# Kernel tuning notes

Measured on AMD Instinct MI355X. Metric: run time of the kernel, lower is better.

The kernel has to match this reference:

```python
import jax, jax.numpy as jnp
import numpy as np

B, N, D, R = 4, 192, 128, 32


def _sh_l1(r):
    # e3nn l=1 real SH with 'integral' normalization: sqrt(3/4pi) * r_hat
    rh = r / (jnp.linalg.norm(r, axis=-1, keepdims=True) + 1e-12)
    return np.sqrt(3.0 / (4.0 * np.pi)).astype(np.float32) * rh


def _sh_l2(r):
    # l=2 real SH of unit vector, integral normalization, standard m=-2..2 order
    rh = r / (jnp.linalg.norm(r, axis=-1, keepdims=True) + 1e-12)
    x, y, z = rh[..., 0], rh[..., 1], rh[..., 2]
    c = np.float32(0.5 / np.sqrt(np.pi))
    s15 = np.float32(np.sqrt(15.0))
    s5h = np.float32(0.5 * np.sqrt(5.0))
    return c * jnp.stack([s15 * x * y, s15 * y * z, s5h * (3.0 * z * z - 1.0),
                          s15 * x * z, 0.5 * s15 * (x * x - y * y)], axis=-1)


def _radial(x, W1, b1, W2, b2):
    return jax.nn.silu(x @ W1 + b1) @ W2 + b2


def _forward(node_s, node_v, node_t, rbf, r_hat, mask,
             Ws1, bs1, Ws2, bs2, Wd1, bd1, Wd2, bd2,
             Wv1, bv1, Wv2, bv2, Wt1, bt1, Wt2, bt2,
             ln_g, ln_b, Wo, bo, v_scale, t_scale):
    m = mask[..., None]                      # (B,N,N,1)
    Y1 = _sh_l1(r_hat)                       # (B,N,N,3)
    Y2 = _sh_l2(r_hat)                       # (B,N,N,5)
    # scalar messages: h_j[b,i,j,d] = node_s[b,j,d]*mask; w0 also masked (mask applied twice, as in source)
    w0 = _radial(rbf, Ws1, bs1, Ws2, bs2) * m
    msg_s = jnp.einsum('bjd,bij,bijd->bid', node_s, mask, w0)
    # vector->scalar channel: source broadcasts node_v over j via unsqueeze(2), i.e. uses node_v of center i
    dot_vY = jnp.einsum('bimd,bijm->bijd', node_v, Y1)     # (B,N,N,D)
    w110 = _radial(rbf, Wd1, bd1, Wd2, bd2) * m
    msg_s_from_v = jnp.sum(dot_vY * w110, axis=2)          # (B,N,D)
    # CG tensor product 0e x SH -> irrep with per-channel radial weight, masked twice
    m2 = (mask * mask)[..., None]
    sj = node_s[:, None, :, :]                             # (B,1,N,D) -> broadcast over i
    wv = _radial(rbf, Wv1, bv1, Wv2, bv2)
    delta_v = jnp.einsum('bijd,bijm->bimd', m2 * wv * sj, Y1)   # (B,N,3,D)
    wt = _radial(rbf, Wt1, bt1, Wt2, bt2)
    delta_t = jnp.einsum('bijd,bijm->bimd', m2 * wt * sj, Y2)   # (B,N,5,D)
    # output scalar head: LayerNorm + Linear
    x = msg_s + msg_s_from_v
    mu = jnp.mean(x, axis=-1, keepdims=True)
    var = jnp.var(x, axis=-1, keepdims=True)
    delta_s = ((x - mu) / jnp.sqrt(var + 1e-5) * ln_g + ln_b) @ Wo + bo
    return delta_s, delta_v * v_scale, delta_t * t_scale


def setup_inputs() -> dict:
    ks = jax.random.split(jax.random.key(0), 16)
    g = lambda i, sh, s=1.0: jax.random.normal(ks[i], sh, jnp.float32) * s
    z = lambda: jnp.zeros((D,), jnp.float32)
    return dict(
        node_s=g(0, (B, N, D)), node_v=g(1, (B, N, 3, D)), node_t=g(2, (B, N, 5, D)),
        rbf=jax.random.uniform(ks[3], (B, N, N, R), jnp.float32),
        r_hat=g(4, (B, N, N, 3)), mask=jnp.ones((B, N, N), jnp.float32),
        Ws1=g(5, (R, D), 0.05), bs1=z(), Ws2=g(6, (D, D), 0.05), bs2=z(),
        Wd1=g(7, (R, D), 0.05), bd1=z(), Wd2=g(8, (D, D), 0.05), bd2=z(),
        Wv1=g(9, (R, D), 0.05), bv1=z(), Wv2=g(10, (D, D), 0.05), bv2=z(),
        Wt1=g(11, (R, D), 0.05), bt1=z(), Wt2=g(12, (D, D), 0.05), bt2=z(),
        ln_g=jnp.ones((D,), jnp.float32), ln_b=z(),
        Wo=g(13, (D, D), 0.05), bo=z(),
        v_scale=jnp.ones((D,), jnp.float32), t_scale=jnp.ones((D,), jnp.float32))


def reference(node_s, node_v, node_t, rbf, r_hat, mask,
              Ws1, bs1, Ws2, bs2, Wd1, bd1, Wd2, bd2,
              Wv1, bv1, Wv2, bv2, Wt1, bt1, Wt2, bt2,
              ln_g, ln_b, Wo, bo, v_scale, t_scale):
    return _forward(node_s, node_v, node_t, rbf, r_hat, mask,
                    Ws1, bs1, Ws2, bs2, Wd1, bd1, Wd2, bd2,
                    Wv1, bv1, Wv2, bv2, Wt1, bt1, Wt2, bt2,
                    ln_g, ln_b, Wo, bo, v_scale, t_scale)
```

## Files before the change

### kernel.cpp

```cpp
#include <hip/hip_runtime.h>
#include <hip/hip_bf16.h>

#define NB 192
#define DD 128
#define RR 32
#define RBS 40
#define SMS 136

typedef __attribute__((ext_vector_type(8))) short bf16x8;
typedef __attribute__((ext_vector_type(4))) float f32x4;

template<int M> struct IC { static constexpr int value = M; };

__device__ __forceinline__ unsigned short f2bf(float x) {
  union { __hip_bfloat16 h; unsigned short u; } c;
  c.h = __float2bfloat16(x);
  return c.u;
}
__device__ __forceinline__ float bf2f(unsigned short u) {
  union { unsigned int u; float f; } c; c.u = ((unsigned int)u) << 16;
  return c.f;
}

__global__ __launch_bounds__(256) void cg_prep(
    const float* __restrict__ Ws1, const float* __restrict__ Wd1,
    const float* __restrict__ Wv1, const float* __restrict__ Wt1,
    const float* __restrict__ Ws2, const float* __restrict__ Wd2,
    const float* __restrict__ Wv2, const float* __restrict__ Wt2,
    const float* __restrict__ bs1, const float* __restrict__ bd1,
    const float* __restrict__ bv1, const float* __restrict__ bt1,
    const float* __restrict__ bs2, const float* __restrict__ bd2,
    const float* __restrict__ bv2, const float* __restrict__ bt2,
    unsigned short* __restrict__ w1f, unsigned short* __restrict__ w2f,
    float* __restrict__ bcat1, float* __restrict__ bcat2)
{
  const float* W1s[4] = {Ws1, Wd1, Wv1, Wt1};
  const float* W2s[4] = {Ws2, Wd2, Wv2, Wt2};
  const float* B1s[4] = {bs1, bd1, bv1, bt1};
  const float* B2s[4] = {bs2, bd2, bv2, bt2};
  int t = blockIdx.x * 256 + threadIdx.x;
  if (t < 2048) {
    int lane = t & 63, f = t >> 6;
    int mlp = f >> 3, htl = f & 7;
    int g = lane >> 4, ln = lane & 15;
    const float* W = W1s[mlp];
    union { unsigned short u[8]; uint4 d; } p;
    #pragma unroll
    for (int e = 0; e < 8; ++e)
      p.u[e] = f2bf(W[(8*g + e) * DD + htl*16 + ln]);
    *(uint4*)&w1f[t * 8] = p.d;
  } else if (t < 10240) {
    int t2 = t - 2048;
    int lane = t2 & 63, f = t2 >> 6;
    int ct = f & 7, ks = (f >> 3) & 3, mlp = f >> 5;
    int g = lane >> 4, ln = lane & 15;
    const float* W = W2s[mlp];
    union { unsigned short u[8]; uint4 d; } p;
    #pragma unroll
    for (int e = 0; e < 8; ++e)
      p.u[e] = f2bf(W[(32*ks + 8*g + e) * DD + ct*16 + ln]);
    *(uint4*)&w2f[t2 * 8] = p.d;
  } else if (t < 10752) {
    int t3 = t - 10240;
    bcat1[t3] = B1s[t3 >> 7][t3 & 127];
  } else if (t < 11264) {
    int t3 = t - 10752;
    bcat2[t3] = B2s[t3 >> 7][t3 & 127];
  }
}

template<int JBLK>
__global__ __launch_bounds__(256, 4) void cg_main(
    const float* __restrict__ node_s, const float* __restrict__ node_v,
    const float* __restrict__ rbf, const float* __restrict__ r_hat,
    const float* __restrict__ mask,
    const unsigned short* __restrict__ w1f, const unsigned short* __restrict__ w2f,
    const float* __restrict__ bcat1, const float* __restrict__ bcat2,
    float* __restrict__ ws)
{
  constexpr int NSPLIT = NB / JBLK;
  constexpr int NT     = JBLK / 16;
  constexpr int RB_B   = JBLK * RBS * 2;
  constexpr int HU_B   = JBLK * 128 * 2;
  constexpr int SM_B   = JBLK * SMS * 2;
  constexpr int YY_B   = 12 * JBLK * 4;
  __shared__ __align__(16) char smem[RB_B + HU_B + SM_B + YY_B];
  unsigned short* Rb  = (unsigned short*)smem;
  unsigned short* Hu  = (unsigned short*)(smem + RB_B);
  unsigned short* SMu = (unsigned short*)(smem + RB_B + HU_B);
  float*          YYf = (float*)(smem + RB_B + HU_B + SM_B);

  const int tid  = threadIdx.x;
  const int bx   = blockIdx.x;
  const int bi   = bx / NSPLIT;
  const int j0   = (bx % NSPLIT) * JBLK;
  const int b    = bi / NB;
  const int wid  = tid >> 6;
  const int lane = tid & 63;
  const int g = lane >> 4, ln = lane & 15;

  auto haddr = [](int j, int hb) {
    return j * 128 + (((hb) ^ ((j & 7) << 4)) >> 1);
  };

  const float* nsb = node_s + (size_t)b * (NB * DD);

  {
    const float4* rrow = (const float4*)(rbf + (size_t)bi * (NB * RR) + j0 * RR);
    #pragma unroll
    for (int f = tid; f < JBLK * 8; f += 256) {
      float4 v = rrow[f];
      union { unsigned short u[4]; uint2 d; } p;
      p.u[0] = f2bf(v.x); p.u[1] = f2bf(v.y); p.u[2] = f2bf(v.z); p.u[3] = f2bf(v.w);
      *(uint2*)&Rb[(f >> 3) * RBS + (f & 7) * 4] = p.d;
    }
  }
  if (tid < JBLK) {
    int jj = j0 + tid;
    const float* rh = r_hat + ((size_t)bi * NB + jj) * 3;
    float x = rh[0], y = rh[1], z = rh[2];
    float m = mask[(size_t)bi * NB + jj];
    float inv = 1.0f / (sqrtf(x*x + y*y + z*z) + 1e-12f);
    x *= inv; y *= inv; z *= inv;
    YYf[ 0*JBLK + tid] = 0.48860252f * m * x;
    YYf[ 1*JBLK + tid] = 0.48860252f * m * y;
    YYf[ 2*JBLK + tid] = 0.48860252f * m * z;
    YYf[ 3*JBLK + tid] = 0.48860252f * x;
    YYf[ 4*JBLK + tid] = 0.48860252f * y;
    YYf[ 5*JBLK + tid] = 0.48860252f * z;
    YYf[ 6*JBLK + tid] = 1.09254843f * x * y;
    YYf[ 7*JBLK + tid] = 1.09254843f * y * z;
    YYf[ 8*JBLK + tid] = 0.31539157f * (3.f * z * z - 1.f);
    YYf[ 9*JBLK + tid] = 1.09254843f * x * z;
    YYf[10*JBLK + tid] = 0.54627422f * (x*x - y*y);
    YYf[11*JBLK + tid] = m * m;
  }
  __syncthreads();

  {
    constexpr int ITER = (JBLK * DD) / 1024;
    #pragma unroll
    for (int i = 0; i < ITER; ++i) {
      int e0 = (i * 256 + tid) * 4;
      int j = e0 >> 7, d0 = e0 & 127;
      float m2 = YYf[11*JBLK + j];
      float4 v = *(const float4*)(nsb + (size_t)(j0 + j) * DD + d0);
      union { unsigned short u[4]; uint2 dq; } p;
      p.u[0] = f2bf(m2*v.x); p.u[1] = f2bf(m2*v.y);
      p.u[2] = f2bf(m2*v.z); p.u[3] = f2bf(m2*v.w);
      *(uint2*)&SMu[j * SMS + d0] = p.dq;
    }
  }

  const int c0 = wid * 32 + ln, c1 = c0 + 16;
  const float* nvb = node_v + (size_t)bi * (3 * DD);
  float V00 = nvb[c0], V10 = nvb[DD + c0], V20 = nvb[2*DD + c0];
  float V01 = nvb[c1], V11 = nvb[DD + c1], V21 = nvb[2*DD + c1];

  float msgs0=0.f, msgs1=0.f, msgsv0=0.f, msgsv1=0.f;
  float dv0x=0,dv0y=0,dv0z=0, dv1x=0,dv1y=0,dv1z=0;
  float dt00=0,dt01=0,dt02=0,dt03=0,dt04=0;
  float dt10=0,dt11=0,dt12=0,dt13=0,dt14=0;

  const f32x4 zacc = {0.f, 0.f, 0.f, 0.f};

  auto do_pass = [&](auto PC) {
    constexpr int MODE = decltype(PC)::value;
    bf16x8 Bf[4][2];
    #pragma unroll
    for (int ks = 0; ks < 4; ++ks)
      #pragma unroll
      for (int t = 0; t < 2; ++t) {
        int f2 = (MODE * 4 + ks) * 8 + 2 * wid + t;
        Bf[ks][t] = *(const bf16x8*)&w2f[(f2 * 64 + lane) * 8];
      }
    float b2c0 = bcat2[MODE * DD + c0], b2c1 = bcat2[MODE * DD + c1];
    #pragma unroll
    for (int q = 0; q < 2; ++q) {
      const int htl = wid * 2 + q;
      const int f   = MODE * 8 + htl;
      bf16x8 a1 = *(const bf16x8*)&w1f[(f * 64 + lane) * 8];
      float4 b1v = *(const float4*)(bcat1 + MODE * DD + htl*16 + 4*g);
      #pragma unroll
      for (int nt = 0; nt < NT; ++nt) {
        int j = nt * 16 + ln;
        bf16x8 bb = *(const bf16x8*)&Rb[j * RBS + 8 * g];
        f32x4 h4 = __builtin_amdgcn_mfma_f32_16x16x32_bf16(a1, bb, zacc, 0, 0, 0);
        union { unsigned short u[4]; uint2 d; } hp;
        float x0 = h4[0] + b1v.x; hp.u[0] = f2bf(x0 * __builtin_amdgcn_rcpf(1.f + __expf(-x0)));
        float x1 = h4[1] + b1v.y; hp.u[1] = f2bf(x1 * __builtin_amdgcn_rcpf(1.f + __expf(-x1)));
        float x2 = h4[2] + b1v.z; hp.u[2] = f2bf(x2 * __builtin_amdgcn_rcpf(1.f + __expf(-x2)));
        float x3 = h4[3] + b1v.w; hp.u[3] = f2bf(x3 * __builtin_amdgcn_rcpf(1.f + __expf(-x3)));
        *(uint2*)&Hu[haddr(j, htl*32 + 8*g)] = hp.d;
      }
    }
    __syncthreads();
    #pragma unroll
    for (int mt = 0; mt < NT; ++mt) {
      int jb = mt * 16;
      f32x4 acc0 = zacc, acc1 = zacc;
      #pragma unroll
      for (int ks = 0; ks < 4; ++ks) {
        bf16x8 a = *(const bf16x8*)&Hu[haddr(jb + ln, ks*64 + 16*g)];
        acc0 = __builtin_amdgcn_mfma_f32_16x16x32_bf16(a, Bf[ks][0], acc0, 0, 0, 0);
        acc1 = __builtin_amdgcn_mfma_f32_16x16x32_bf16(a, Bf[ks][1], acc1, 0, 0, 0);
      }
      #pragma unroll
      for (int r = 0; r < 4; ++r) {
        int j = jb + 4*g + r;
        float w0 = acc0[r] + b2c0, w1 = acc1[r] + b2c1;
        if constexpr (MODE == 0) {
          float s0 = bf2f(SMu[j*SMS + c0]), s1 = bf2f(SMu[j*SMS + c1]);
          msgs0 += s0 * w0; msgs1 += s1 * w1;
        } else if constexpr (MODE == 1) {
          float yx = YYf[0*JBLK + j], yy = YYf[1*JBLK + j], yz = YYf[2*JBLK + j];
          msgsv0 += (V00*yx + V10*yy + V20*yz) * w0;
          msgsv1 += (V01*yx + V11*yy + V21*yz) * w1;
        } else if constexpr (MODE == 2) {
          float yx = YYf[3*JBLK + j], yy = YYf[4*JBLK + j], yz = YYf[5*JBLK + j];
          float s0 = bf2f(SMu[j*SMS + c0]), s1 = bf2f(SMu[j*SMS + c1]);
          float t0 = s0 * w0, t1 = s1 * w1;
          dv0x += t0*yx; dv0y += t0*yy; dv0z += t0*yz;
          dv1x += t1*yx; dv1y += t1*yy; dv1z += t1*yz;
        } else {
          float ya = YYf[6*JBLK + j], yb = YYf[7*JBLK + j], yc = YYf[8*JBLK + j];
          float yd = YYf[9*JBLK + j], ye = YYf[10*JBLK + j];
          float s0 = bf2f(SMu[j*SMS + c0]), s1 = bf2f(SMu[j*SMS + c1]);
          float t0 = s0 * w0, t1 = s1 * w1;
          dt00 += t0*ya; dt01 += t0*yb; dt02 += t0*yc; dt03 += t0*yd; dt04 += t0*ye;
          dt10 += t1*ya; dt11 += t1*yb; dt12 += t1*yc; dt13 += t1*yd; dt14 += t1*ye;
        }
      }
    }
    __syncthreads();
  };

  do_pass(IC<0>{});
  do_pass(IC<1>{});
  do_pass(IC<2>{});
  do_pass(IC<3>{});

  auto wred = [](float v) { v += __shfl_xor(v, 16); v += __shfl_xor(v, 32); return v; };
  float q0[10] = {msgs0, msgsv0, dv0x, dv0y, dv0z, dt00, dt01, dt02, dt03, dt04};
  float q1[10] = {msgs1, msgsv1, dv1x, dv1y, dv1z, dt10, dt11, dt12, dt13, dt14};
  #pragma unroll
  for (int k = 0; k < 10; ++k) { q0[k] = wred(q0[k]); q1[k] = wred(q1[k]); }
  if (g == 0) {
    float* w0 = ws + (size_t)bx * 1280;
    #pragma unroll
    for (int k = 0; k < 10; ++k) {
      w0[k*128 + c0] = q0[k];
      w0[k*128 + c1] = q1[k];
    }
  }
}

template<int NSPLIT>
__global__ __launch_bounds__(256) void cg_final(
    const float* __restrict__ ws,
    const float* __restrict__ ln_g, const float* __restrict__ ln_b,
    const float* __restrict__ Wo, const float* __restrict__ bo,
    const float* __restrict__ v_scale, const float* __restrict__ t_scale,
    float* __restrict__ out)
{
  __shared__ float Xv[128];
  __shared__ float XN[128];
  __shared__ float PS[2][128];
  __shared__ float ST[2];
  const int bi = blockIdx.x;
  const int tid = threadIdx.x;

  if (tid < 128) {
    float acc[10];
    #pragma unroll
    for (int k = 0; k < 10; ++k) acc[k] = 0.f;
    #pragma unroll
    for (int q = 0; q < NSPLIT; ++q) {
      const float* pa = ws + ((size_t)bi * NSPLIT + q) * 1280;
      #pragma unroll
      for (int k = 0; k < 10; ++k) acc[k] += pa[k*128 + tid];
    }
    float vs = v_scale[tid], ts = t_scale[tid];
    size_t vbase = 98304 + (size_t)bi * (3 * DD) + tid;
    out[vbase]        = acc[2] * vs;
    out[vbase + DD]   = acc[3] * vs;
    out[vbase + 2*DD] = acc[4] * vs;
    size_t tbase = 393216 + (size_t)bi * (5 * DD) + tid;
    out[tbase]        = acc[5] * ts;
    out[tbase + DD]   = acc[6] * ts;
    out[tbase + 2*DD] = acc[7] * ts;
    out[tbase + 3*DD] = acc[8] * ts;
    out[tbase + 4*DD] = acc[9] * ts;
    Xv[tid] = acc[0] + acc[1];
  }
  __syncthreads();
  if (tid < 64) {
    float a = Xv[tid], c = Xv[tid + 64];
    float s = a + c, ss = a*a + c*c;
    #pragma unroll
    for (int off = 32; off > 0; off >>= 1) {
      s  += __shfl_down(s, off);
      ss += __shfl_down(ss, off);
    }
    if (tid == 0) {
      float mu  = s * (1.f / 128.f);
      float var = ss * (1.f / 128.f) - mu * mu;
      ST[0] = mu; ST[1] = rsqrtf(var + 1e-5f);
    }
  }
  __syncthreads();
  if (tid < 128) XN[tid] = (Xv[tid] - ST[0]) * ST[1] * ln_g[tid] + ln_b[tid];
  __syncthreads();
  {
    int dp = tid & 127, p = tid >> 7;
    float s = 0.f;
    #pragma unroll
    for (int dd = 0; dd < 64; ++dd) {
      int d = p * 64 + dd;
      s += XN[d] * Wo[d * DD + dp];
    }
    PS[p][dp] = s;
  }
  __syncthreads();
  if (tid < 128)
    out[(size_t)bi * DD + tid] = PS[0][tid] + PS[1][tid] + bo[tid];
}

extern "C" void kernel_launch(void* const* d_in, const int* in_sizes, int n_in,
                              void* d_out, int out_size, void* d_ws, size_t ws_size,
                              hipStream_t stream) {
  (void)in_sizes; (void)n_in; (void)out_size;
  const float* node_s = (const float*)d_in[0];
  const float* node_v = (const float*)d_in[1];
  const float* rbf    = (const float*)d_in[3];
  const float* r_hat  = (const float*)d_in[4];
  const float* mask   = (const float*)d_in[5];
  const float* Ws1 = (const float*)d_in[6];  const float* bs1 = (const float*)d_in[7];
  const float* Ws2 = (const float*)d_in[8];  const float* bs2 = (const float*)d_in[9];
  const float* Wd1 = (const float*)d_in[10]; const float* bd1 = (const float*)d_in[11];
  const float* Wd2 = (const float*)d_in[12]; const float* bd2 = (const float*)d_in[13];
  const float* Wv1 = (const float*)d_in[14]; const float* bv1 = (const float*)d_in[15];
  const float* Wv2 = (const float*)d_in[16]; const float* bv2 = (const float*)d_in[17];
  const float* Wt1 = (const float*)d_in[18]; const float* bt1 = (const float*)d_in[19];
  const float* Wt2 = (const float*)d_in[20]; const float* bt2 = (const float*)d_in[21];
  const float* ln_g = (const float*)d_in[22]; const float* ln_b = (const float*)d_in[23];
  const float* Wo   = (const float*)d_in[24]; const float* bo   = (const float*)d_in[25];
  const float* v_scale = (const float*)d_in[26];
  const float* t_scale = (const float*)d_in[27];
  float* outp = (float*)d_out;

  const size_t wtail = 16384ull*2 + 65536ull*2 + 1024ull*4;
  const size_t need4 = 3072ull * 1280 * 4 + wtail;
  char* wsb = (char*)d_ws;

  bool use4 = (ws_size >= need4);
  size_t pbytes = use4 ? 3072ull * 1280 * 4 : 1536ull * 1280 * 4;
  float* partials = (float*)wsb;
  unsigned short* w1f = (unsigned short*)(wsb + pbytes);
  unsigned short* w2f = w1f + 16384;
  float* bcat1 = (float*)(w2f + 65536);
  float* bcat2 = bcat1 + 512;

  hipLaunchKernelGGL(cg_prep, dim3(44), dim3(256), 0, stream,
                     Ws1, Wd1, Wv1, Wt1, Ws2, Wd2, Wv2, Wt2,
                     bs1, bd1, bv1, bt1, bs2, bd2, bv2, bt2,
                     w1f, w2f, bcat1, bcat2);

  if (use4) {
    hipLaunchKernelGGL((cg_main<48>), dim3(4 * 768), dim3(256), 0, stream,
                       node_s, node_v, rbf, r_hat, mask,
                       w1f, w2f, bcat1, bcat2, partials);
    hipLaunchKernelGGL((cg_final<4>), dim3(768), dim3(256), 0, stream,
                       partials, ln_g, ln_b, Wo, bo, v_scale, t_scale, outp);
  } else {
    hipLaunchKernelGGL((cg_main<96>), dim3(2 * 768), dim3(256), 0, stream,
                       node_s, node_v, rbf, r_hat, mask,
                       w1f, w2f, bcat1, bcat2, partials);
    hipLaunchKernelGGL((cg_final<2>), dim3(768), dim3(256), 0, stream,
                       partials, ln_g, ln_b, Wo, bo, v_scale, t_scale, outp);
  }
}
```

Before: 74.08 us.

## Split the four radial-MLP passes across separate blocks by mode

```diff
diff --git a/kernel.cpp b/kernel.cpp
--- a/kernel.cpp
+++ b/kernel.cpp
@@ -70,7 +70,7 @@
 }
 
 template<int JBLK>
-__global__ __launch_bounds__(256, 4) void cg_main(
+__global__ __launch_bounds__(256, 5) void cg_main(
     const float* __restrict__ node_s, const float* __restrict__ node_v,
     const float* __restrict__ rbf, const float* __restrict__ r_hat,
     const float* __restrict__ mask,
@@ -83,8 +83,7 @@
   constexpr int RB_B   = JBLK * RBS * 2;
   constexpr int HU_B   = JBLK * 128 * 2;
   constexpr int SM_B   = JBLK * SMS * 2;
-  constexpr int YY_B   = 12 * JBLK * 4;
-  __shared__ __align__(16) char smem[RB_B + HU_B + SM_B + YY_B];
+  __shared__ __align__(16) char smem[RB_B + HU_B + SM_B + 6 * JBLK * 4];
   unsigned short* Rb  = (unsigned short*)smem;
   unsigned short* Hu  = (unsigned short*)(smem + RB_B);
   unsigned short* SMu = (unsigned short*)(smem + RB_B + HU_B);
@@ -92,8 +91,10 @@
 
   const int tid  = threadIdx.x;
   const int bx   = blockIdx.x;
-  const int bi   = bx / NSPLIT;
-  const int j0   = (bx % NSPLIT) * JBLK;
+  const int mode = bx & 3;
+  const int jq   = (bx >> 2) % NSPLIT;
+  const int bi   = bx / (4 * NSPLIT);
+  const int j0   = jq * JBLK;
   const int b    = bi / NB;
   const int wid  = tid >> 6;
   const int lane = tid & 63;
@@ -104,77 +105,72 @@
   };
 
   const float* nsb = node_s + (size_t)b * (NB * DD);
-
-  {
-    const float4* rrow = (const float4*)(rbf + (size_t)bi * (NB * RR) + j0 * RR);
-    #pragma unroll
-    for (int f = tid; f < JBLK * 8; f += 256) {
-      float4 v = rrow[f];
-      union { unsigned short u[4]; uint2 d; } p;
-      p.u[0] = f2bf(v.x); p.u[1] = f2bf(v.y); p.u[2] = f2bf(v.z); p.u[3] = f2bf(v.w);
-      *(uint2*)&Rb[(f >> 3) * RBS + (f & 7) * 4] = p.d;
-    }
-  }
-  if (tid < JBLK) {
-    int jj = j0 + tid;
-    const float* rh = r_hat + ((size_t)bi * NB + jj) * 3;
-    float x = rh[0], y = rh[1], z = rh[2];
-    float m = mask[(size_t)bi * NB + jj];
-    float inv = 1.0f / (sqrtf(x*x + y*y + z*z) + 1e-12f);
-    x *= inv; y *= inv; z *= inv;
-    YYf[ 0*JBLK + tid] = 0.48860252f * m * x;
-    YYf[ 1*JBLK + tid] = 0.48860252f * m * y;
-    YYf[ 2*JBLK + tid] = 0.48860252f * m * z;
-    YYf[ 3*JBLK + tid] = 0.48860252f * x;
-    YYf[ 4*JBLK + tid] = 0.48860252f * y;
-    YYf[ 5*JBLK + tid] = 0.48860252f * z;
-    YYf[ 6*JBLK + tid] = 1.09254843f * x * y;
-    YYf[ 7*JBLK + tid] = 1.09254843f * y * z;
-    YYf[ 8*JBLK + tid] = 0.31539157f * (3.f * z * z - 1.f);
-    YYf[ 9*JBLK + tid] = 1.09254843f * x * z;
-    YYf[10*JBLK + tid] = 0.54627422f * (x*x - y*y);
-    YYf[11*JBLK + tid] = m * m;
-  }
-  __syncthreads();
-
-  {
-    constexpr int ITER = (JBLK * DD) / 1024;
-    #pragma unroll
-    for (int i = 0; i < ITER; ++i) {
-      int e0 = (i * 256 + tid) * 4;
-      int j = e0 >> 7, d0 = e0 & 127;
-      float m2 = YYf[11*JBLK + j];
-      float4 v = *(const float4*)(nsb + (size_t)(j0 + j) * DD + d0);
-      union { unsigned short u[4]; uint2 dq; } p;
-      p.u[0] = f2bf(m2*v.x); p.u[1] = f2bf(m2*v.y);
-      p.u[2] = f2bf(m2*v.z); p.u[3] = f2bf(m2*v.w);
-      *(uint2*)&SMu[j * SMS + d0] = p.dq;
-    }
-  }
-
-  const int c0 = wid * 32 + ln, c1 = c0 + 16;
   const float* nvb = node_v + (size_t)bi * (3 * DD);
-  float V00 = nvb[c0], V10 = nvb[DD + c0], V20 = nvb[2*DD + c0];
-  float V01 = nvb[c1], V11 = nvb[DD + c1], V21 = nvb[2*DD + c1];
-
-  float msgs0=0.f, msgs1=0.f, msgsv0=0.f, msgsv1=0.f;
-  float dv0x=0,dv0y=0,dv0z=0, dv1x=0,dv1y=0,dv1z=0;
-  float dt00=0,dt01=0,dt02=0,dt03=0,dt04=0;
-  float dt10=0,dt11=0,dt12=0,dt13=0,dt14=0;
-
   const f32x4 zacc = {0.f, 0.f, 0.f, 0.f};
 
-  auto do_pass = [&](auto PC) {
-    constexpr int MODE = decltype(PC)::value;
-    bf16x8 Bf[4][2];
-    #pragma unroll
-    for (int ks = 0; ks < 4; ++ks)
+  auto run = [&](auto MC) {
+    constexpr int MODE = decltype(MC)::value;
+    constexpr int NK   = (MODE == 3) ? 5 : (MODE == 2) ? 3 : 1;
+    constexpr int P0   = (MODE == 0) ? 0 : (MODE == 1) ? 1 : (MODE == 2) ? 2 : 5;
+
+    float Vv[3][2];
+    if constexpr (MODE == 1) {
       #pragma unroll
       for (int t = 0; t < 2; ++t) {
-        int f2 = (MODE * 4 + ks) * 8 + 2 * wid + t;
-        Bf[ks][t] = *(const bf16x8*)&w2f[(f2 * 64 + lane) * 8];
-      }
-    float b2c0 = bcat2[MODE * DD + c0], b2c1 = bcat2[MODE * DD + c1];
+        int c = (wid * 2 + t) * 16 + ln;
+        Vv[0][t] = nvb[c]; Vv[1][t] = nvb[DD + c]; Vv[2][t] = nvb[2*DD + c];
+      }
+    }
+
+    {
+      const float4* rrow = (const float4*)(rbf + (size_t)bi * (NB * RR) + j0 * RR);
+      #pragma unroll
+      for (int f = tid; f < JBLK * 8; f += 256) {
+        float4 v = rrow[f];
+        union { unsigned short u[4]; uint2 d; } p;
+        p.u[0] = f2bf(v.x); p.u[1] = f2bf(v.y); p.u[2] = f2bf(v.z); p.u[3] = f2bf(v.w);
+        *(uint2*)&Rb[(f >> 3) * RBS + (f & 7) * 4] = p.d;
+      }
+    }
+    if (tid < JBLK) {
+      int jj = j0 + tid;
+      const float* rh = r_hat + ((size_t)bi * NB + jj) * 3;
+      float x = rh[0], y = rh[1], z = rh[2];
+      float m = mask[(size_t)bi * NB + jj];
+      float inv = 1.0f / (sqrtf(x*x + y*y + z*z) + 1e-12f);
+      x *= inv; y *= inv; z *= inv;
+      YYf[tid] = m * m;
+      if constexpr (MODE == 1) {
+        YYf[1*JBLK + tid] = 0.48860252f * m * x;
+        YYf[2*JBLK + tid] = 0.48860252f * m * y;
+        YYf[3*JBLK + tid] = 0.48860252f * m * z;
+      } else if constexpr (MODE == 2) {
+        YYf[1*JBLK + tid] = 0.48860252f * x;
+        YYf[2*JBLK + tid] = 0.48860252f * y;
+        YYf[3*JBLK + tid] = 0.48860252f * z;
+      } else if constexpr (MODE == 3) {
+        YYf[1*JBLK + tid] = 1.09254843f * x * y;
+        YYf[2*JBLK + tid] = 1.09254843f * y * z;
+        YYf[3*JBLK + tid] = 0.31539157f * (3.f * z * z - 1.f);
+        YYf[4*JBLK + tid] = 1.09254843f * x * z;
+        YYf[5*JBLK + tid] = 0.54627422f * (x*x - y*y);
+      }
+    }
+    __syncthreads();
+
+    if constexpr (MODE != 1) {
+      #pragma unroll
+      for (int i = 0; i < (JBLK * DD) / 1024; ++i) {
+        int e0 = (i * 256 + tid) * 4;
+        int j = e0 >> 7, d0 = e0 & 127;
+        float m2 = YYf[j];
+        float4 v = *(const float4*)(nsb + (size_t)(j0 + j) * DD + d0);
+        union { unsigned short u[4]; uint2 dq; } p;
+        p.u[0] = f2bf(m2*v.x); p.u[1] = f2bf(m2*v.y);
+        p.u[2] = f2bf(m2*v.z); p.u[3] = f2bf(m2*v.w);
+        *(uint2*)&SMu[j * SMS + d0] = p.dq;
+      }
+    }
     #pragma unroll
     for (int q = 0; q < 2; ++q) {
       const int htl = wid * 2 + q;
@@ -195,63 +191,75 @@
       }
     }
     __syncthreads();
-    #pragma unroll
-    for (int mt = 0; mt < NT; ++mt) {
-      int jb = mt * 16;
-      f32x4 acc0 = zacc, acc1 = zacc;
-      #pragma unroll
-      for (int ks = 0; ks < 4; ++ks) {
-        bf16x8 a = *(const bf16x8*)&Hu[haddr(jb + ln, ks*64 + 16*g)];
-        acc0 = __builtin_amdgcn_mfma_f32_16x16x32_bf16(a, Bf[ks][0], acc0, 0, 0, 0);
-        acc1 = __builtin_amdgcn_mfma_f32_16x16x32_bf16(a, Bf[ks][1], acc1, 0, 0, 0);
-      }
-      #pragma unroll
-      for (int r = 0; r < 4; ++r) {
-        int j = jb + 4*g + r;
-        float w0 = acc0[r] + b2c0, w1 = acc1[r] + b2c1;
-        if constexpr (MODE == 0) {
-          float s0 = bf2f(SMu[j*SMS + c0]), s1 = bf2f(SMu[j*SMS + c1]);
-          msgs0 += s0 * w0; msgs1 += s1 * w1;
-        } else if constexpr (MODE == 1) {
-          float yx = YYf[0*JBLK + j], yy = YYf[1*JBLK + j], yz = YYf[2*JBLK + j];
-          msgsv0 += (V00*yx + V10*yy + V20*yz) * w0;
-          msgsv1 += (V01*yx + V11*yy + V21*yz) * w1;
-        } else if constexpr (MODE == 2) {
-          float yx = YYf[3*JBLK + j], yy = YYf[4*JBLK + j], yz = YYf[5*JBLK + j];
-          float s0 = bf2f(SMu[j*SMS + c0]), s1 = bf2f(SMu[j*SMS + c1]);
-          float t0 = s0 * w0, t1 = s1 * w1;
-          dv0x += t0*yx; dv0y += t0*yy; dv0z += t0*yz;
-          dv1x += t1*yx; dv1y += t1*yy; dv1z += t1*yz;
-        } else {
-          float ya = YYf[6*JBLK + j], yb = YYf[7*JBLK + j], yc = YYf[8*JBLK + j];
-          float yd = YYf[9*JBLK + j], ye = YYf[10*JBLK + j];
-          float s0 = bf2f(SMu[j*SMS + c0]), s1 = bf2f(SMu[j*SMS + c1]);
-          float t0 = s0 * w0, t1 = s1 * w1;
-          dt00 += t0*ya; dt01 += t0*yb; dt02 += t0*yc; dt03 += t0*yd; dt04 += t0*ye;
-          dt10 += t1*ya; dt11 += t1*yb; dt12 += t1*yc; dt13 += t1*yd; dt14 += t1*ye;
+
+    float ak[NK][2];
+    #pragma unroll
+    for (int k = 0; k < NK; ++k) { ak[k][0] = 0.f; ak[k][1] = 0.f; }
+
+    #pragma unroll
+    for (int t = 0; t < 2; ++t) {
+      const int ct = wid * 2 + t;
+      const int c  = ct * 16 + ln;
+      bf16x8 Bf[4];
+      #pragma unroll
+      for (int ks = 0; ks < 4; ++ks)
+        Bf[ks] = *(const bf16x8*)&w2f[(((MODE*4 + ks)*8 + ct) * 64 + lane) * 8];
+      float b2c = bcat2[MODE * DD + c];
+      #pragma unroll
+      for (int mt = 0; mt < NT; ++mt) {
+        f32x4 acc = zacc;
+        #pragma unroll
+        for (int ks = 0; ks < 4; ++ks) {
+          bf16x8 a = *(const bf16x8*)&Hu[haddr(mt*16 + ln, ks*64 + 16*g)];
+          acc = __builtin_amdgcn_mfma_f32_16x16x32_bf16(a, Bf[ks], acc, 0, 0, 0);
         }
-      }
-    }
-    __syncthreads();
+        #pragma unroll
+        for (int r = 0; r < 4; ++r) {
+          int j = mt*16 + 4*g + r;
+          float w = acc[r] + b2c;
+          if constexpr (MODE == 0) {
+            ak[0][t] += bf2f(SMu[j*SMS + c]) * w;
+          } else if constexpr (MODE == 1) {
+            ak[0][t] += (Vv[0][t]*YYf[1*JBLK + j] + Vv[1][t]*YYf[2*JBLK + j]
+                       + Vv[2][t]*YYf[3*JBLK + j]) * w;
+          } else if constexpr (MODE == 2) {
+            float p = bf2f(SMu[j*SMS + c]) * w;
+            ak[0][t] += p * YYf[1*JBLK + j];
+            ak[1][t] += p * YYf[2*JBLK + j];
+            ak[2][t] += p * YYf[3*JBLK + j];
+          } else {
+            float p = bf2f(SMu[j*SMS + c]) * w;
+            ak[0][t] += p * YYf[1*JBLK + j];
+            ak[1][t] += p * YYf[2*JBLK + j];
+            ak[2][t] += p * YYf[3*JBLK + j];
+            ak[3][t] += p * YYf[4*JBLK + j];
+            ak[4][t] += p * YYf[5*JBLK + j];
+          }
+        }
+      }
+    }
+
+    auto wred = [](float v) { v += __shfl_xor(v, 16); v += __shfl_xor(v, 32); return v; };
+    #pragma unroll
+    for (int k = 0; k < NK; ++k) {
+      ak[k][0] = wred(ak[k][0]);
+      ak[k][1] = wred(ak[k][1]);
+    }
+    if (g == 0) {
+      float* slab = ws + ((size_t)bi * NSPLIT + jq) * 1280;
+      #pragma unroll
+      for (int k = 0; k < NK; ++k) {
+        slab[(P0 + k)*128 + (wid*2 + 0)*16 + ln] = ak[k][0];
+        slab[(P0 + k)*128 + (wid*2 + 1)*16 + ln] = ak[k][1];
+      }
+    }
   };
 
-  do_pass(IC<0>{});
-  do_pass(IC<1>{});
-  do_pass(IC<2>{});
-  do_pass(IC<3>{});
-
-  auto wred = [](float v) { v += __shfl_xor(v, 16); v += __shfl_xor(v, 32); return v; };
-  float q0[10] = {msgs0, msgsv0, dv0x, dv0y, dv0z, dt00, dt01, dt02, dt03, dt04};
-  float q1[10] = {msgs1, msgsv1, dv1x, dv1y, dv1z, dt10, dt11, dt12, dt13, dt14};
-  #pragma unroll
-  for (int k = 0; k < 10; ++k) { q0[k] = wred(q0[k]); q1[k] = wred(q1[k]); }
-  if (g == 0) {
-    float* w0 = ws + (size_t)bx * 1280;
-    #pragma unroll
-    for (int k = 0; k < 10; ++k) {
-      w0[k*128 + c0] = q0[k];
-      w0[k*128 + c1] = q1[k];
-    }
+  switch (mode) {
+    case 0: run(IC<0>{}); break;
+    case 1: run(IC<1>{}); break;
+    case 2: run(IC<2>{}); break;
+    default: run(IC<3>{}); break;
   }
 }
 
@@ -350,11 +358,11 @@
   float* outp = (float*)d_out;
 
   const size_t wtail = 16384ull*2 + 65536ull*2 + 1024ull*4;
-  const size_t need4 = 3072ull * 1280 * 4 + wtail;
+  const size_t need4 = 768ull * 4 * 1280 * 4 + wtail;
   char* wsb = (char*)d_ws;
 
   bool use4 = (ws_size >= need4);
-  size_t pbytes = use4 ? 3072ull * 1280 * 4 : 1536ull * 1280 * 4;
+  size_t pbytes = use4 ? 768ull * 4 * 1280 * 4 : 768ull * 2 * 1280 * 4;
   float* partials = (float*)wsb;
   unsigned short* w1f = (unsigned short*)(wsb + pbytes);
   unsigned short* w2f = w1f + 16384;
@@ -367,13 +375,13 @@
                      w1f, w2f, bcat1, bcat2);
 
   if (use4) {
-    hipLaunchKernelGGL((cg_main<48>), dim3(4 * 768), dim3(256), 0, stream,
+    hipLaunchKernelGGL((cg_main<48>), dim3(768 * 4 * 4), dim3(256), 0, stream,
                        node_s, node_v, rbf, r_hat, mask,
                        w1f, w2f, bcat1, bcat2, partials);
     hipLaunchKernelGGL((cg_final<4>), dim3(768), dim3(256), 0, stream,
                        partials, ln_g, ln_b, Wo, bo, v_scale, t_scale, outp);
   } else {
-    hipLaunchKernelGGL((cg_main<96>), dim3(2 * 768), dim3(256), 0, stream,
+    hipLaunchKernelGGL((cg_main<96>), dim3(768 * 2 * 4), dim3(256), 0, stream,
                        node_s, node_v, rbf, r_hat, mask,
                        w1f, w2f, bcat1, bcat2, partials);
     hipLaunchKernelGGL((cg_final<2>), dim3(768), dim3(256), 0, stream,
```

Measured after the change: 99.37 us. 1.34x slower.

## Move per-j spherical-harmonic reductions onto MFMA and retile to 64-neighbor blocks

Applied to the files above, without the earlier changes.

```diff
diff --git a/kernel.cpp b/kernel.cpp
--- a/kernel.cpp
+++ b/kernel.cpp
@@ -5,7 +5,7 @@
 #define DD 128
 #define RR 32
 #define RBS 40
-#define SMS 136
+#define SMS 132
 
 typedef __attribute__((ext_vector_type(8))) short bf16x8;
 typedef __attribute__((ext_vector_type(4))) float f32x4;
@@ -20,6 +20,10 @@
 __device__ __forceinline__ float bf2f(unsigned short u) {
   union { unsigned int u; float f; } c; c.u = ((unsigned int)u) << 16;
   return c.f;
+}
+__device__ __forceinline__ unsigned int pack2bf(float a, float b) {
+  union { unsigned short u[2]; unsigned int w; } r;
+  r.u[0] = f2bf(a); r.u[1] = f2bf(b); return r.w;
 }
 
 __global__ __launch_bounds__(256) void cg_prep(
@@ -70,7 +74,7 @@
 }
 
 template<int JBLK>
-__global__ __launch_bounds__(256, 4) void cg_main(
+__global__ __launch_bounds__(256, 3) void cg_main(
     const float* __restrict__ node_s, const float* __restrict__ node_v,
     const float* __restrict__ rbf, const float* __restrict__ r_hat,
     const float* __restrict__ mask,
@@ -80,20 +84,24 @@
 {
   constexpr int NSPLIT = NB / JBLK;
   constexpr int NT     = JBLK / 16;
+  constexpr int KSL    = JBLK / 32;
   constexpr int RB_B   = JBLK * RBS * 2;
   constexpr int HU_B   = JBLK * 128 * 2;
   constexpr int SM_B   = JBLK * SMS * 2;
   constexpr int YY_B   = 12 * JBLK * 4;
-  __shared__ __align__(16) char smem[RB_B + HU_B + SM_B + YY_B];
+  constexpr int YA_B   = 4 * KSL * 64 * 16;
+  __shared__ __align__(16) char smem[RB_B + HU_B + SM_B + YY_B + YA_B];
   unsigned short* Rb  = (unsigned short*)smem;
   unsigned short* Hu  = (unsigned short*)(smem + RB_B);
   unsigned short* SMu = (unsigned short*)(smem + RB_B + HU_B);
   float*          YYf = (float*)(smem + RB_B + HU_B + SM_B);
+  unsigned short* YA  = (unsigned short*)(smem + RB_B + HU_B + SM_B + YY_B);
 
   const int tid  = threadIdx.x;
   const int bx   = blockIdx.x;
   const int bi   = bx / NSPLIT;
-  const int j0   = (bx % NSPLIT) * JBLK;
+  const int jq   = bx % NSPLIT;
+  const int j0   = jq * JBLK;
   const int b    = bi / NB;
   const int wid  = tid >> 6;
   const int lane = tid & 63;
@@ -104,6 +112,7 @@
   };
 
   const float* nsb = node_s + (size_t)b * (NB * DD);
+  const f32x4 zacc = {0.f, 0.f, 0.f, 0.f};
 
   {
     const float4* rrow = (const float4*)(rbf + (size_t)bi * (NB * RR) + j0 * RR);
@@ -122,58 +131,69 @@
     float m = mask[(size_t)bi * NB + jj];
     float inv = 1.0f / (sqrtf(x*x + y*y + z*z) + 1e-12f);
     x *= inv; y *= inv; z *= inv;
-    YYf[ 0*JBLK + tid] = 0.48860252f * m * x;
-    YYf[ 1*JBLK + tid] = 0.48860252f * m * y;
-    YYf[ 2*JBLK + tid] = 0.48860252f * m * z;
-    YYf[ 3*JBLK + tid] = 0.48860252f * x;
-    YYf[ 4*JBLK + tid] = 0.48860252f * y;
-    YYf[ 5*JBLK + tid] = 0.48860252f * z;
-    YYf[ 6*JBLK + tid] = 1.09254843f * x * y;
-    YYf[ 7*JBLK + tid] = 1.09254843f * y * z;
-    YYf[ 8*JBLK + tid] = 0.31539157f * (3.f * z * z - 1.f);
-    YYf[ 9*JBLK + tid] = 1.09254843f * x * z;
-    YYf[10*JBLK + tid] = 0.54627422f * (x*x - y*y);
-    YYf[11*JBLK + tid] = m * m;
-  }
-  __syncthreads();
-
-  {
-    constexpr int ITER = (JBLK * DD) / 1024;
-    #pragma unroll
-    for (int i = 0; i < ITER; ++i) {
-      int e0 = (i * 256 + tid) * 4;
-      int j = e0 >> 7, d0 = e0 & 127;
-      float m2 = YYf[11*JBLK + j];
-      float4 v = *(const float4*)(nsb + (size_t)(j0 + j) * DD + d0);
-      union { unsigned short u[4]; uint2 dq; } p;
-      p.u[0] = f2bf(m2*v.x); p.u[1] = f2bf(m2*v.y);
-      p.u[2] = f2bf(m2*v.z); p.u[3] = f2bf(m2*v.w);
-      *(uint2*)&SMu[j * SMS + d0] = p.dq;
-    }
+    YYf[ 0*JBLK + tid] = m * m;
+    YYf[ 1*JBLK + tid] = 0.48860252f * m * x;
+    YYf[ 2*JBLK + tid] = 0.48860252f * m * y;
+    YYf[ 3*JBLK + tid] = 0.48860252f * m * z;
+    YYf[ 4*JBLK + tid] = 0.48860252f * x;
+    YYf[ 5*JBLK + tid] = 0.48860252f * y;
+    YYf[ 6*JBLK + tid] = 0.48860252f * z;
+    YYf[ 7*JBLK + tid] = 1.09254843f * x * y;
+    YYf[ 8*JBLK + tid] = 1.09254843f * y * z;
+    YYf[ 9*JBLK + tid] = 0.31539157f * (3.f * z * z - 1.f);
+    YYf[10*JBLK + tid] = 1.09254843f * x * z;
+    YYf[11*JBLK + tid] = 0.54627422f * (x*x - y*y);
+  }
+  __syncthreads();
+
+  #pragma unroll
+  for (int i = 0; i < (JBLK * DD) / 1024; ++i) {
+    int e0 = (i * 256 + tid) * 4;
+    int j = e0 >> 7, d0 = e0 & 127;
+    float m2 = YYf[j];
+    float4 v = *(const float4*)(nsb + (size_t)(j0 + j) * DD + d0);
+    union { unsigned short u[4]; uint2 dq; } p;
+    p.u[0] = f2bf(m2*v.x); p.u[1] = f2bf(m2*v.y);
+    p.u[2] = f2bf(m2*v.z); p.u[3] = f2bf(m2*v.w);
+    *(uint2*)&SMu[j * SMS + d0] = p.dq;
+  }
+  for (int s = tid; s < 4 * KSL * 64; s += 256) {
+    int lane_l = s & 63, rest = s >> 6;
+    int ksl = rest % KSL, m = rest / KSL;
+    int gl = lane_l >> 4, lnl = lane_l & 15;
+    int jb0 = 32*ksl + 4*gl;
+    union { unsigned short u[8]; uint4 d; } P;
+    bool ok = (m == 1 && lnl >= 1 && lnl <= 3) ||
+              (m == 2 && lnl >= 4 && lnl <= 6) ||
+              (m == 3 && lnl >= 7 && lnl <= 11);
+    if (m == 0) {
+      unsigned short one = (lnl == 0) ? (unsigned short)0x3F80 : (unsigned short)0;
+      #pragma unroll
+      for (int e = 0; e < 8; ++e) P.u[e] = one;
+    } else if (ok) {
+      const float* pl = YYf + lnl * JBLK;
+      float4 a = *(const float4*)(pl + jb0);
+      float4 c = *(const float4*)(pl + jb0 + 16);
+      P.u[0]=f2bf(a.x); P.u[1]=f2bf(a.y); P.u[2]=f2bf(a.z); P.u[3]=f2bf(a.w);
+      P.u[4]=f2bf(c.x); P.u[5]=f2bf(c.y); P.u[6]=f2bf(c.z); P.u[7]=f2bf(c.w);
+    } else {
+      #pragma unroll
+      for (int e = 0; e < 8; ++e) P.u[e] = 0;
+    }
+    *(uint4*)&YA[s * 8] = P.d;
   }
 
   const int c0 = wid * 32 + ln, c1 = c0 + 16;
-  const float* nvb = node_v + (size_t)bi * (3 * DD);
-  float V00 = nvb[c0], V10 = nvb[DD + c0], V20 = nvb[2*DD + c0];
-  float V01 = nvb[c1], V11 = nvb[DD + c1], V21 = nvb[2*DD + c1];
-
-  float msgs0=0.f, msgs1=0.f, msgsv0=0.f, msgsv1=0.f;
-  float dv0x=0,dv0y=0,dv0z=0, dv1x=0,dv1y=0,dv1z=0;
-  float dt00=0,dt01=0,dt02=0,dt03=0,dt04=0;
-  float dt10=0,dt11=0,dt12=0,dt13=0,dt14=0;
-
-  const f32x4 zacc = {0.f, 0.f, 0.f, 0.f};
-
-  auto do_pass = [&](auto PC) {
-    constexpr int MODE = decltype(PC)::value;
+  f32x4 accY0 = zacc, accY1 = zacc;
+
+  auto run = [&](auto MC) {
+    constexpr int MODE = decltype(MC)::value;
     bf16x8 Bf[4][2];
     #pragma unroll
     for (int ks = 0; ks < 4; ++ks)
       #pragma unroll
-      for (int t = 0; t < 2; ++t) {
-        int f2 = (MODE * 4 + ks) * 8 + 2 * wid + t;
-        Bf[ks][t] = *(const bf16x8*)&w2f[(f2 * 64 + lane) * 8];
-      }
+      for (int t = 0; t < 2; ++t)
+        Bf[ks][t] = *(const bf16x8*)&w2f[(((MODE*4 + ks)*8 + 2*wid + t) * 64 + lane) * 8];
     float b2c0 = bcat2[MODE * DD + c0], b2c1 = bcat2[MODE * DD + c1];
     #pragma unroll
     for (int q = 0; q < 2; ++q) {
@@ -195,69 +215,66 @@
       }
     }
     __syncthreads();
+    unsigned int pw[2][NT][2];
     #pragma unroll
     for (int mt = 0; mt < NT; ++mt) {
-      int jb = mt * 16;
       f32x4 acc0 = zacc, acc1 = zacc;
       #pragma unroll
       for (int ks = 0; ks < 4; ++ks) {
-        bf16x8 a = *(const bf16x8*)&Hu[haddr(jb + ln, ks*64 + 16*g)];
+        bf16x8 a = *(const bf16x8*)&Hu[haddr(mt*16 + ln, ks*64 + 16*g)];
         acc0 = __builtin_amdgcn_mfma_f32_16x16x32_bf16(a, Bf[ks][0], acc0, 0, 0, 0);
         acc1 = __builtin_amdgcn_mfma_f32_16x16x32_bf16(a, Bf[ks][1], acc1, 0, 0, 0);
       }
       #pragma unroll
-      for (int r = 0; r < 4; ++r) {
-        int j = jb + 4*g + r;
-        float w0 = acc0[r] + b2c0, w1 = acc1[r] + b2c1;
-        if constexpr (MODE == 0) {
-          float s0 = bf2f(SMu[j*SMS + c0]), s1 = bf2f(SMu[j*SMS + c1]);
-          msgs0 += s0 * w0; msgs1 += s1 * w1;
-        } else if constexpr (MODE == 1) {
-          float yx = YYf[0*JBLK + j], yy = YYf[1*JBLK + j], yz = YYf[2*JBLK + j];
-          msgsv0 += (V00*yx + V10*yy + V20*yz) * w0;
-          msgsv1 += (V01*yx + V11*yy + V21*yz) * w1;
-        } else if constexpr (MODE == 2) {
-          float yx = YYf[3*JBLK + j], yy = YYf[4*JBLK + j], yz = YYf[5*JBLK + j];
-          float s0 = bf2f(SMu[j*SMS + c0]), s1 = bf2f(SMu[j*SMS + c1]);
-          float t0 = s0 * w0, t1 = s1 * w1;
-          dv0x += t0*yx; dv0y += t0*yy; dv0z += t0*yz;
-          dv1x += t1*yx; dv1y += t1*yy; dv1z += t1*yz;
+      for (int wd = 0; wd < 2; ++wd) {
+        int jl = mt*16 + 4*g + 2*wd;
+        float w00 = acc0[2*wd] + b2c0, w01 = acc0[2*wd+1] + b2c0;
+        float w10 = acc1[2*wd] + b2c1, w11 = acc1[2*wd+1] + b2c1;
+        float p00, p01, p10, p11;
+        if constexpr (MODE == 1) {
+          p00 = w00; p01 = w01; p10 = w10; p11 = w11;
         } else {
-          float ya = YYf[6*JBLK + j], yb = YYf[7*JBLK + j], yc = YYf[8*JBLK + j];
-          float yd = YYf[9*JBLK + j], ye = YYf[10*JBLK + j];
-          float s0 = bf2f(SMu[j*SMS + c0]), s1 = bf2f(SMu[j*SMS + c1]);
-          float t0 = s0 * w0, t1 = s1 * w1;
-          dt00 += t0*ya; dt01 += t0*yb; dt02 += t0*yc; dt03 += t0*yd; dt04 += t0*ye;
-          dt10 += t1*ya; dt11 += t1*yb; dt12 += t1*yc; dt13 += t1*yd; dt14 += t1*ye;
+          p00 = bf2f(SMu[jl*SMS + c0]) * w00;
+          p01 = bf2f(SMu[(jl+1)*SMS + c0]) * w01;
+          p10 = bf2f(SMu[jl*SMS + c1]) * w10;
+          p11 = bf2f(SMu[(jl+1)*SMS + c1]) * w11;
         }
+        pw[0][mt][wd] = pack2bf(p00, p01);
+        pw[1][mt][wd] = pack2bf(p10, p11);
       }
+    }
+    #pragma unroll
+    for (int ksl = 0; ksl < KSL; ++ksl) {
+      bf16x8 ya = *(const bf16x8*)&YA[((MODE*KSL + ksl) * 64 + lane) * 8];
+      union { bf16x8 v; unsigned int w[4]; } B0, B1;
+      B0.w[0] = pw[0][2*ksl][0]; B0.w[1] = pw[0][2*ksl][1];
+      B0.w[2] = pw[0][2*ksl+1][0]; B0.w[3] = pw[0][2*ksl+1][1];
+      B1.w[0] = pw[1][2*ksl][0]; B1.w[1] = pw[1][2*ksl][1];
+      B1.w[2] = pw[1][2*ksl+1][0]; B1.w[3] = pw[1][2*ksl+1][1];
+      accY0 = __builtin_amdgcn_mfma_f32_16x16x32_bf16(ya, B0.v, accY0, 0, 0, 0);
+      accY1 = __builtin_amdgcn_mfma_f32_16x16x32_bf16(ya, B1.v, accY1, 0, 0, 0);
     }
     __syncthreads();
   };
 
-  do_pass(IC<0>{});
-  do_pass(IC<1>{});
-  do_pass(IC<2>{});
-  do_pass(IC<3>{});
-
-  auto wred = [](float v) { v += __shfl_xor(v, 16); v += __shfl_xor(v, 32); return v; };
-  float q0[10] = {msgs0, msgsv0, dv0x, dv0y, dv0z, dt00, dt01, dt02, dt03, dt04};
-  float q1[10] = {msgs1, msgsv1, dv1x, dv1y, dv1z, dt10, dt11, dt12, dt13, dt14};
-  #pragma unroll
-  for (int k = 0; k < 10; ++k) { q0[k] = wred(q0[k]); q1[k] = wred(q1[k]); }
-  if (g == 0) {
-    float* w0 = ws + (size_t)bx * 1280;
-    #pragma unroll
-    for (int k = 0; k < 10; ++k) {
-      w0[k*128 + c0] = q0[k];
-      w0[k*128 + c1] = q1[k];
+  run(IC<0>{});
+  run(IC<1>{});
+  run(IC<2>{});
+  run(IC<3>{});
+
+  if (g < 3) {
+    float* slab = ws + ((size_t)bi * NSPLIT + jq) * (12 * 128);
+    #pragma unroll
+    for (int r = 0; r < 4; ++r) {
+      slab[(4*g + r) * 128 + c0] = accY0[r];
+      slab[(4*g + r) * 128 + c1] = accY1[r];
     }
   }
 }
 
 template<int NSPLIT>
 __global__ __launch_bounds__(256) void cg_final(
-    const float* __restrict__ ws,
+    const float* __restrict__ ws, const float* __restrict__ node_v,
     const float* __restrict__ ln_g, const float* __restrict__ ln_b,
     const float* __restrict__ Wo, const float* __restrict__ bo,
     const float* __restrict__ v_scale, const float* __restrict__ t_scale,
@@ -271,27 +288,29 @@
   const int tid = threadIdx.x;
 
   if (tid < 128) {
-    float acc[10];
-    #pragma unroll
-    for (int k = 0; k < 10; ++k) acc[k] = 0.f;
+    float acc[12];
+    #pragma unroll
+    for (int k = 0; k < 12; ++k) acc[k] = 0.f;
     #pragma unroll
     for (int q = 0; q < NSPLIT; ++q) {
-      const float* pa = ws + ((size_t)bi * NSPLIT + q) * 1280;
-      #pragma unroll
-      for (int k = 0; k < 10; ++k) acc[k] += pa[k*128 + tid];
-    }
+      const float* pa = ws + ((size_t)bi * NSPLIT + q) * (12 * 128);
+      #pragma unroll
+      for (int k = 0; k < 12; ++k) acc[k] += pa[k*128 + tid];
+    }
+    const float* nvb = node_v + (size_t)bi * (3 * DD) + tid;
+    float x = acc[0] + nvb[0]*acc[1] + nvb[DD]*acc[2] + nvb[2*DD]*acc[3];
     float vs = v_scale[tid], ts = t_scale[tid];
     size_t vbase = 98304 + (size_t)bi * (3 * DD) + tid;
-    out[vbase]        = acc[2] * vs;
-    out[vbase + DD]   = acc[3] * vs;
-    out[vbase + 2*DD] = acc[4] * vs;
+    out[vbase]        = acc[4] * vs;
+    out[vbase + DD]   = acc[5] * vs;
+    out[vbase + 2*DD] = acc[6] * vs;
     size_t tbase = 393216 + (size_t)bi * (5 * DD) + tid;
-    out[tbase]        = acc[5] * ts;
-    out[tbase + DD]   = acc[6] * ts;
-    out[tbase + 2*DD] = acc[7] * ts;
-    out[tbase + 3*DD] = acc[8] * ts;
-    out[tbase + 4*DD] = acc[9] * ts;
-    Xv[tid] = acc[0] + acc[1];
+    out[tbase]        = acc[7]  * ts;
+    out[tbase + DD]   = acc[8]  * ts;
+    out[tbase + 2*DD] = acc[9]  * ts;
+    out[tbase + 3*DD] = acc[10] * ts;
+    out[tbase + 4*DD] = acc[11] * ts;
+    Xv[tid] = x;
   }
   __syncthreads();
   if (tid < 64) {
@@ -329,7 +348,7 @@
 extern "C" void kernel_launch(void* const* d_in, const int* in_sizes, int n_in,
                               void* d_out, int out_size, void* d_ws, size_t ws_size,
                               hipStream_t stream) {
-  (void)in_sizes; (void)n_in; (void)out_size;
+  (void)in_sizes; (void)n_in; (void)out_size; (void)ws_size;
   const float* node_s = (const float*)d_in[0];
   const float* node_v = (const float*)d_in[1];
   const float* rbf    = (const float*)d_in[3];
@@ -349,12 +368,8 @@
   const float* t_scale = (const float*)d_in[27];
   float* outp = (float*)d_out;
 
-  const size_t wtail = 16384ull*2 + 65536ull*2 + 1024ull*4;
-  const size_t need4 = 3072ull * 1280 * 4 + wtail;
+  const size_t pbytes = 768ull * 3 * 1536 * 4;
   char* wsb = (char*)d_ws;
-
-  bool use4 = (ws_size >= need4);
-  size_t pbytes = use4 ? 3072ull * 1280 * 4 : 1536ull * 1280 * 4;
   float* partials = (float*)wsb;
   unsigned short* w1f = (unsigned short*)(wsb + pbytes);
   unsigned short* w2f = w1f + 16384;
@@ -366,17 +381,9 @@
                      bs1, bd1, bv1, bt1, bs2, bd2, bv2, bt2,
                      w1f, w2f, bcat1, bcat2);
 
-  if (use4) {
-    hipLaunchKernelGGL((cg_main<48>), dim3(4 * 768), dim3(256), 0, stream,
-                       node_s, node_v, rbf, r_hat, mask,
-                       w1f, w2f, bcat1, bcat2, partials);
-    hipLaunchKernelGGL((cg_final<4>), dim3(768), dim3(256), 0, stream,
-                       partials, ln_g, ln_b, Wo, bo, v_scale, t_scale, outp);
-  } else {
-    hipLaunchKernelGGL((cg_main<96>), dim3(2 * 768), dim3(256), 0, stream,
-                       node_s, node_v, rbf, r_hat, mask,
-                       w1f, w2f, bcat1, bcat2, partials);
-    hipLaunchKernelGGL((cg_final<2>), dim3(768), dim3(256), 0, stream,
-                       partials, ln_g, ln_b, Wo, bo, v_scale, t_scale, outp);
-  }
-}
+  hipLaunchKernelGGL((cg_main<64>), dim3(768 * 3), dim3(256), 0, stream,
+                     node_s, node_v, rbf, r_hat, mask,
+                     w1f, w2f, bcat1, bcat2, partials);
+  hipLaunchKernelGGL((cg_final<3>), dim3(768), dim3(256), 0, stream,
+                     partials, node_v, ln_g, ln_b, Wo, bo, v_scale, t_scale, outp);
+}
```

After: 64.78 us. -12.6%, faster.
